# Kernel optimization log

Measured on AMD Instinct MI355X. Metric: run time of the kernel, lower is better.

## Reference

```python
import jax, jax.numpy as jnp
import numpy as np

EPS = 1e-12  # matches torch F.normalize default eps

def setup_inputs() -> dict:
    key = jax.random.key(0)
    k1, k2 = jax.random.split(key)
    n, d = 8192, 1024
    x = jax.random.normal(k1, (n, d), dtype=jnp.float32)
    weight = jax.random.normal(k2, (d, d), dtype=jnp.float32) * (2.0 / d) ** 0.5
    return {"x": x, "weight": weight}

def reference(x, weight):
    # L2-normalize rows (torch F.normalize, dim=1): x / max(||x||_2, eps)
    nrm = jnp.sqrt(jnp.sum(x * x, axis=1, keepdims=True))
    norm = x / jnp.maximum(nrm, EPS)
    # adjacency: cosine-similarity Gram matrix [n, n] (materialized as in source)
    adj = norm @ norm.T
    ax = adj @ x          # [n, d]
    axw = ax @ weight     # [n, d]
    return axw
```

## Files before the change

kernel.cpp:

```cpp
#include <hip/hip_runtime.h>
#include <stdint.h>

typedef unsigned short u16;
typedef unsigned int u32;
typedef __attribute__((ext_vector_type(8))) short short8;
typedef __attribute__((ext_vector_type(4))) float floatx4;

__device__ __forceinline__ u16 f2b(float f) {
    u32 u = __builtin_bit_cast(u32, f);
    return (u16)((u + 0x7fffu + ((u >> 16) & 1u)) >> 16);
}

__device__ __forceinline__ void gld16(const void* g, void* l) {
    __builtin_amdgcn_global_load_lds(
        (const __attribute__((address_space(1))) u32*)g,
        (__attribute__((address_space(3))) u32*)l, 16, 0, 0);
}

__global__ __launch_bounds__(256) void prep_norms(
    const float* __restrict__ x, float* __restrict__ rnorm, float* __restrict__ srnorm) {
    int row = blockIdx.x;
    int t = threadIdx.x;
    float4 v = ((const float4*)(x + (long)row * 1024))[t];
    float ss = v.x * v.x + v.y * v.y + v.z * v.z + v.w * v.w;
    #pragma unroll
    for (int off = 32; off > 0; off >>= 1) ss += __shfl_down(ss, off);
    __shared__ float red[4];
    if ((t & 63) == 0) red[t >> 6] = ss;
    __syncthreads();
    if (t == 0) {
        float r = 1.0f / fmaxf(sqrtf(red[0] + red[1] + red[2] + red[3]), 1e-12f);
        rnorm[row] = r;
        srnorm[row] = sqrtf(r);
    }
}

__global__ __launch_bounds__(256) void transpose_scale_dual(
    const float* __restrict__ src, const float* __restrict__ sr,
    u16* __restrict__ dstT, u16* __restrict__ dstR, int rows, int cols) {
    __shared__ float tile[64][65];
    __shared__ float rbuf[64];
    int r0 = blockIdx.x * 64, c0 = blockIdx.y * 64;
    int t = threadIdx.x;
    if (t < 64) rbuf[t] = (sr != nullptr) ? sr[r0 + t] : 1.0f;
    __syncthreads();
    #pragma unroll
    for (int i = 0; i < 4; i++) {
        int lin = i * 256 + t;
        int rr = lin >> 4, c4 = (lin & 15) << 2;
        float4 v = *(const float4*)(src + (long)(r0 + rr) * cols + c0 + c4);
        float s = rbuf[rr];
        v.x *= s; v.y *= s; v.z *= s; v.w *= s;
        tile[rr][c4] = v.x; tile[rr][c4 + 1] = v.y; tile[rr][c4 + 2] = v.z; tile[rr][c4 + 3] = v.w;
        if (dstR != nullptr) {
            ushort4 o; o.x = f2b(v.x); o.y = f2b(v.y); o.z = f2b(v.z); o.w = f2b(v.w);
            *(ushort4*)(dstR + (long)(r0 + rr) * cols + c0 + c4) = o;
        }
    }
    __syncthreads();
    #pragma unroll
    for (int i = 0; i < 4; i++) {
        int lin = i * 256 + t;
        int cc = lin >> 4, r4 = (lin & 15) << 2;
        ushort4 o;
        o.x = f2b(tile[r4][cc]);
        o.y = f2b(tile[r4 + 1][cc]);
        o.z = f2b(tile[r4 + 2][cc]);
        o.w = f2b(tile[r4 + 3][cc]);
        *(ushort4*)(dstT + (long)(c0 + cc) * rows + r0 + r4) = o;
    }
}

__global__ __launch_bounds__(256) void reduce_cast(
    const float* __restrict__ P, u16* __restrict__ D, int S, long E) {
    long i = ((long)blockIdx.x * 256 + threadIdx.x) * 4;
    float4 s = *(const float4*)(P + i);
    for (int z = 1; z < S; z++) {
        float4 v = *(const float4*)(P + z * E + i);
        s.x += v.x; s.y += v.y; s.z += v.z; s.w += v.w;
    }
    ushort4 o;
    o.x = f2b(s.x); o.y = f2b(s.y); o.z = f2b(s.z); o.w = f2b(s.w);
    *(ushort4*)(D + i) = o;
}

__global__ __launch_bounds__(256) void reduce_sym64(
    const float* __restrict__ P, u16* __restrict__ D, int S, long E) {
    __shared__ float lt[64][65];
    int ti = blockIdx.x >> 4, tj = blockIdx.x & 15;
    int t = threadIdx.x;
    int r = t >> 4, c4 = (t & 15) << 2;
    int kept = (ti <= 2 * (tj >> 1) + 1);
    if (kept) {
        #pragma unroll
        for (int it = 0; it < 4; it++) {
            int row = 64 * ti + it * 16 + r;
            long idx = (long)row * 1024 + 64 * tj + c4;
            float4 s = *(const float4*)(P + idx);
            for (int z = 1; z < S; z++) {
                float4 v = *(const float4*)(P + (long)z * E + idx);
                s.x += v.x; s.y += v.y; s.z += v.z; s.w += v.w;
            }
            ushort4 o; o.x = f2b(s.x); o.y = f2b(s.y); o.z = f2b(s.z); o.w = f2b(s.w);
            *(ushort4*)(D + idx) = o;
        }
    } else {
        #pragma unroll
        for (int it = 0; it < 4; it++) {
            int row = it * 16 + r;
            long idx = (long)(64 * tj + row) * 1024 + 64 * ti + c4;
            float4 s = *(const float4*)(P + idx);
            for (int z = 1; z < S; z++) {
                float4 v = *(const float4*)(P + (long)z * E + idx);
                s.x += v.x; s.y += v.y; s.z += v.z; s.w += v.w;
            }
            lt[row][c4] = s.x; lt[row][c4 + 1] = s.y; lt[row][c4 + 2] = s.z; lt[row][c4 + 3] = s.w;
        }
        __syncthreads();
        #pragma unroll
        for (int it = 0; it < 4; it++) {
            int dr = it * 16 + r;
            ushort4 o;
            o.x = f2b(lt[c4 + 0][dr]); o.y = f2b(lt[c4 + 1][dr]);
            o.z = f2b(lt[c4 + 2][dr]); o.w = f2b(lt[c4 + 3][dr]);
            *(ushort4*)(D + (long)(64 * ti + dr) * 1024 + 64 * tj + c4) = o;
        }
    }
}

__global__ __launch_bounds__(256, 4) void gemm64x128(
    const u16* __restrict__ A, const u16* __restrict__ B,
    float* __restrict__ C, const float* __restrict__ rowscale,
    int lda, int ldb, int ldc, int tilesN, int kIters, long coffz, int sym) {
    __shared__ __align__(16) u16 As[64 * 64];
    __shared__ __align__(16) u16 Bs[128 * 64];
    int tm, tn;
    if (sym) {
        int id = blockIdx.x, j = 0;
        while (true) {
            int c = (2 * j + 2 < 16) ? (2 * j + 2) : 16;
            if (id < c) break;
            id -= c; j++;
        }
        tn = j; tm = id;
    } else {
        tm = blockIdx.x / tilesN; tn = blockIdx.x % tilesN;
    }
    long kOff = (long)blockIdx.y * kIters * 64;
    const u16* Ap = A + (long)tm * 64 * lda + kOff;
    const u16* Bp = B + (long)tn * 128 * ldb + kOff;
    long coff = (long)blockIdx.y * coffz;

    int t = threadIdx.x;
    int lane = t & 63, w = t >> 6;
    int wm = (w & 1) * 32, wn = (w >> 1) * 64;
    int r16 = lane & 15, q = lane >> 4;

    int acl[2], bcl[4];
    #pragma unroll
    for (int j = 0; j < 2; j++) acl[j] = (w * 2 + j) * 64 + lane;
    #pragma unroll
    for (int j = 0; j < 4; j++) bcl[j] = (w * 4 + j) * 64 + lane;

    floatx4 acc[2][4];
    #pragma unroll
    for (int i = 0; i < 2; i++)
        #pragma unroll
        for (int j = 0; j < 4; j++) acc[i][j] = (floatx4){0.f, 0.f, 0.f, 0.f};

    for (int kt = 0; kt < kIters; kt++) {
        long kk = (long)kt * 64;
        #pragma unroll
        for (int j = 0; j < 2; j++) {
            int cl = acl[j], row = cl >> 3, cg = (cl & 7) ^ (row & 7);
            gld16(Ap + (long)row * lda + kk + cg * 8, (void*)&As[cl * 8]);
        }
        #pragma unroll
        for (int j = 0; j < 4; j++) {
            int cl = bcl[j], row = cl >> 3, cg = (cl & 7) ^ (row & 7);
            gld16(Bp + (long)row * ldb + kk + cg * 8, (void*)&Bs[cl * 8]);
        }
        __syncthreads();
        #pragma unroll
        for (int ks = 0; ks < 2; ks++) {
            short8 a[2], b[4];
            #pragma unroll
            for (int i = 0; i < 2; i++) {
                int rr = wm + i * 16 + r16;
                int cc = (ks * 4 + q) ^ (rr & 7);
                a[i] = *(const short8*)&As[rr * 64 + cc * 8];
            }
            #pragma unroll
            for (int j = 0; j < 4; j++) {
                int rr = wn + j * 16 + r16;
                int cc = (ks * 4 + q) ^ (rr & 7);
                b[j] = *(const short8*)&Bs[rr * 64 + cc * 8];
            }
            #pragma unroll
            for (int i = 0; i < 2; i++)
                #pragma unroll
                for (int j = 0; j < 4; j++)
                    acc[i][j] = __builtin_amdgcn_mfma_f32_16x16x32_bf16(a[i], b[j], acc[i][j], 0, 0, 0);
        }
        __syncthreads();
    }

    int m0 = tm * 64 + wm, n0 = tn * 128 + wn;
    #pragma unroll
    for (int i = 0; i < 2; i++) {
        int mm = m0 + i * 16 + q * 4;
        float rs[4];
        #pragma unroll
        for (int r = 0; r < 4; r++) rs[r] = (rowscale != nullptr) ? rowscale[mm + r] : 1.0f;
        #pragma unroll
        for (int j = 0; j < 4; j++) {
            int nn = n0 + j * 16 + r16;
            #pragma unroll
            for (int r = 0; r < 4; r++)
                C[coff + (long)(mm + r) * ldc + nn] = acc[i][j][r] * rs[r];
        }
    }
}

extern "C" void kernel_launch(void* const* d_in, const int* in_sizes, int n_in,
                              void* d_out, int out_size, void* d_ws, size_t ws_size,
                              hipStream_t stream) {
    const float* x = (const float*)d_in[0];
    const float* wgt = (const float*)d_in[1];
    float* out = (float*)d_out;
    char* ws = (char*)d_ws;

    const size_t MB = 1048576;
    float* rnorm  = (float*)ws;
    float* srnorm = (float*)(ws + 32768);
    u16*   YT     = (u16*)(ws + 65536);
    u16*   Yb     = (u16*)(ws + 65536 + 16 * MB);
    u16*   Wt     = (u16*)(ws + 65536 + 32 * MB);
    u16*   Gb     = (u16*)(ws + 65536 + 34 * MB);
    u16*   Mt     = (u16*)(ws + 65536 + 36 * MB);
    float* Gp     = (float*)(ws + 65536 + 38 * MB);
    float* Mp     = (float*)(ws + 65536 + 70 * MB);

    prep_norms<<<8192, 256, 0, stream>>>(x, rnorm, srnorm);
    transpose_scale_dual<<<dim3(128, 16), 256, 0, stream>>>(x, srnorm, YT, Yb, 8192, 1024);
    transpose_scale_dual<<<dim3(16, 16), 256, 0, stream>>>(wgt, nullptr, Wt, nullptr, 1024, 1024);
    gemm64x128<<<dim3(72, 8), 256, 0, stream>>>(YT, YT, Gp, nullptr,
                                                8192, 8192, 1024, 8, 16, 1048576, 1);
    reduce_sym64<<<256, 256, 0, stream>>>(Gp, Gb, 8, 1048576);
    gemm64x128<<<dim3(128, 2), 256, 0, stream>>>(Wt, Gb, Mp, nullptr,
                                                 1024, 1024, 1024, 8, 8, 1048576, 0);
    reduce_cast<<<1024, 256, 0, stream>>>(Mp, Mt, 2, 1048576);
    gemm64x128<<<dim3(1024, 1), 256, 0, stream>>>(Yb, Mt, out, srnorm,
                                                  1024, 1024, 1024, 8, 16, 0, 0);
}
```

Before: 167.6 us.

## Fuse prep kernels, store split-K partials in bf16, double split-K factors

Merges the norm computation, the bf16 cast of x and the weight transpose into a single prep kernel. The scaled transpose now reads the bf16 copy instead of the fp32 input. The split-K GEMMs write bf16 partials instead of fp32, halving partial traffic, and double their split counts (16 for the Gram matrix, 4 for W·G) to raise parallelism. The final GEMM uses the unscaled bf16 x with the full reciprocal norm as its row scale. Rounding partials to bf16 before summing adds precision loss.

After: 177.0 us. 5.6% more time.

```diff
diff --git a/kernel.cpp b/kernel.cpp
--- a/kernel.cpp
+++ b/kernel.cpp
@@ -10,52 +10,79 @@
     u32 u = __builtin_bit_cast(u32, f);
     return (u16)((u + 0x7fffu + ((u >> 16) & 1u)) >> 16);
 }
-
+__device__ __forceinline__ float b2f(u16 b) {
+    u32 u = ((u32)b) << 16;
+    return __builtin_bit_cast(float, u);
+}
 __device__ __forceinline__ void gld16(const void* g, void* l) {
     __builtin_amdgcn_global_load_lds(
         (const __attribute__((address_space(1))) u32*)g,
         (__attribute__((address_space(3))) u32*)l, 16, 0, 0);
 }
 
-__global__ __launch_bounds__(256) void prep_norms(
-    const float* __restrict__ x, float* __restrict__ rnorm, float* __restrict__ srnorm) {
-    int row = blockIdx.x;
-    int t = threadIdx.x;
-    float4 v = ((const float4*)(x + (long)row * 1024))[t];
-    float ss = v.x * v.x + v.y * v.y + v.z * v.z + v.w * v.w;
-    #pragma unroll
-    for (int off = 32; off > 0; off >>= 1) ss += __shfl_down(ss, off);
-    __shared__ float red[4];
-    if ((t & 63) == 0) red[t >> 6] = ss;
-    __syncthreads();
-    if (t == 0) {
-        float r = 1.0f / fmaxf(sqrtf(red[0] + red[1] + red[2] + red[3]), 1e-12f);
-        rnorm[row] = r;
-        srnorm[row] = sqrtf(r);
-    }
-}
-
-__global__ __launch_bounds__(256) void transpose_scale_dual(
-    const float* __restrict__ src, const float* __restrict__ sr,
-    u16* __restrict__ dstT, u16* __restrict__ dstR, int rows, int cols) {
+__global__ __launch_bounds__(256) void prep_all(
+    const float* __restrict__ x, const float* __restrict__ wgt,
+    float* __restrict__ rnorm, float* __restrict__ srnorm,
+    u16* __restrict__ xb, u16* __restrict__ Wt) {
     __shared__ float tile[64][65];
-    __shared__ float rbuf[64];
+    int bid = blockIdx.x;
+    int t = threadIdx.x;
+    if (bid < 8192) {
+        float4 v = ((const float4*)(x + (long)bid * 1024))[t];
+        float ss = v.x * v.x + v.y * v.y + v.z * v.z + v.w * v.w;
+        #pragma unroll
+        for (int off = 32; off > 0; off >>= 1) ss += __shfl_down(ss, off);
+        if ((t & 63) == 0) tile[0][t >> 6] = ss;
+        __syncthreads();
+        if (t == 0) {
+            float r = 1.0f / fmaxf(sqrtf(tile[0][0] + tile[0][1] + tile[0][2] + tile[0][3]), 1e-12f);
+            rnorm[bid] = r;
+            srnorm[bid] = sqrtf(r);
+        }
+        ushort4 o;
+        o.x = f2b(v.x); o.y = f2b(v.y); o.z = f2b(v.z); o.w = f2b(v.w);
+        *(ushort4*)(xb + (long)bid * 1024 + t * 4) = o;
+    } else {
+        int b2 = bid - 8192;
+        int r0 = (b2 >> 4) * 64, c0 = (b2 & 15) * 64;
+        #pragma unroll
+        for (int i = 0; i < 4; i++) {
+            int lin = i * 256 + t;
+            int rr = lin >> 4, c4 = (lin & 15) << 2;
+            float4 v = *(const float4*)(wgt + (long)(r0 + rr) * 1024 + c0 + c4);
+            tile[rr][c4] = v.x; tile[rr][c4 + 1] = v.y; tile[rr][c4 + 2] = v.z; tile[rr][c4 + 3] = v.w;
+        }
+        __syncthreads();
+        #pragma unroll
+        for (int i = 0; i < 4; i++) {
+            int lin = i * 256 + t;
+            int cc = lin >> 4, r4 = (lin & 15) << 2;
+            ushort4 o;
+            o.x = f2b(tile[r4][cc]);     o.y = f2b(tile[r4 + 1][cc]);
+            o.z = f2b(tile[r4 + 2][cc]); o.w = f2b(tile[r4 + 3][cc]);
+            *(ushort4*)(Wt + (long)(c0 + cc) * 1024 + r0 + r4) = o;
+        }
+    }
+}
+
+__global__ __launch_bounds__(256) void transpose_xb(
+    const u16* __restrict__ xb, const float* __restrict__ sr, u16* __restrict__ YT) {
+    __shared__ u16 tile[64][72];
+    __shared__ float rb[64];
     int r0 = blockIdx.x * 64, c0 = blockIdx.y * 64;
     int t = threadIdx.x;
-    if (t < 64) rbuf[t] = (sr != nullptr) ? sr[r0 + t] : 1.0f;
+    if (t < 64) rb[t] = sr[r0 + t];
     __syncthreads();
     #pragma unroll
     for (int i = 0; i < 4; i++) {
         int lin = i * 256 + t;
         int rr = lin >> 4, c4 = (lin & 15) << 2;
-        float4 v = *(const float4*)(src + (long)(r0 + rr) * cols + c0 + c4);
-        float s = rbuf[rr];
-        v.x *= s; v.y *= s; v.z *= s; v.w *= s;
-        tile[rr][c4] = v.x; tile[rr][c4 + 1] = v.y; tile[rr][c4 + 2] = v.z; tile[rr][c4 + 3] = v.w;
-        if (dstR != nullptr) {
-            ushort4 o; o.x = f2b(v.x); o.y = f2b(v.y); o.z = f2b(v.z); o.w = f2b(v.w);
-            *(ushort4*)(dstR + (long)(r0 + rr) * cols + c0 + c4) = o;
-        }
+        ushort4 v = *(const ushort4*)(xb + (long)(r0 + rr) * 1024 + c0 + c4);
+        float s = rb[rr];
+        tile[rr][c4]     = f2b(b2f(v.x) * s);
+        tile[rr][c4 + 1] = f2b(b2f(v.y) * s);
+        tile[rr][c4 + 2] = f2b(b2f(v.z) * s);
+        tile[rr][c4 + 3] = f2b(b2f(v.w) * s);
     }
     __syncthreads();
     #pragma unroll
@@ -63,29 +90,14 @@
         int lin = i * 256 + t;
         int cc = lin >> 4, r4 = (lin & 15) << 2;
         ushort4 o;
-        o.x = f2b(tile[r4][cc]);
-        o.y = f2b(tile[r4 + 1][cc]);
-        o.z = f2b(tile[r4 + 2][cc]);
-        o.w = f2b(tile[r4 + 3][cc]);
-        *(ushort4*)(dstT + (long)(c0 + cc) * rows + r0 + r4) = o;
-    }
-}
-
-__global__ __launch_bounds__(256) void reduce_cast(
-    const float* __restrict__ P, u16* __restrict__ D, int S, long E) {
-    long i = ((long)blockIdx.x * 256 + threadIdx.x) * 4;
-    float4 s = *(const float4*)(P + i);
-    for (int z = 1; z < S; z++) {
-        float4 v = *(const float4*)(P + z * E + i);
-        s.x += v.x; s.y += v.y; s.z += v.z; s.w += v.w;
-    }
-    ushort4 o;
-    o.x = f2b(s.x); o.y = f2b(s.y); o.z = f2b(s.z); o.w = f2b(s.w);
-    *(ushort4*)(D + i) = o;
-}
-
-__global__ __launch_bounds__(256) void reduce_sym64(
-    const float* __restrict__ P, u16* __restrict__ D, int S, long E) {
+        o.x = tile[r4][cc]; o.y = tile[r4 + 1][cc];
+        o.z = tile[r4 + 2][cc]; o.w = tile[r4 + 3][cc];
+        *(ushort4*)(YT + (long)(c0 + cc) * 8192 + r0 + r4) = o;
+    }
+}
+
+__global__ __launch_bounds__(256) void reduce_sym64_b16(
+    const u16* __restrict__ P, u16* __restrict__ D, int S, long E) {
     __shared__ float lt[64][65];
     int ti = blockIdx.x >> 4, tj = blockIdx.x & 15;
     int t = threadIdx.x;
@@ -96,12 +108,12 @@
         for (int it = 0; it < 4; it++) {
             int row = 64 * ti + it * 16 + r;
             long idx = (long)row * 1024 + 64 * tj + c4;
-            float4 s = *(const float4*)(P + idx);
-            for (int z = 1; z < S; z++) {
-                float4 v = *(const float4*)(P + (long)z * E + idx);
-                s.x += v.x; s.y += v.y; s.z += v.z; s.w += v.w;
-            }
-            ushort4 o; o.x = f2b(s.x); o.y = f2b(s.y); o.z = f2b(s.z); o.w = f2b(s.w);
+            float s0 = 0, s1 = 0, s2 = 0, s3 = 0;
+            for (int z = 0; z < S; z++) {
+                ushort4 v = *(const ushort4*)(P + (long)z * E + idx);
+                s0 += b2f(v.x); s1 += b2f(v.y); s2 += b2f(v.z); s3 += b2f(v.w);
+            }
+            ushort4 o; o.x = f2b(s0); o.y = f2b(s1); o.z = f2b(s2); o.w = f2b(s3);
             *(ushort4*)(D + idx) = o;
         }
     } else {
@@ -109,12 +121,12 @@
         for (int it = 0; it < 4; it++) {
             int row = it * 16 + r;
             long idx = (long)(64 * tj + row) * 1024 + 64 * ti + c4;
-            float4 s = *(const float4*)(P + idx);
-            for (int z = 1; z < S; z++) {
-                float4 v = *(const float4*)(P + (long)z * E + idx);
-                s.x += v.x; s.y += v.y; s.z += v.z; s.w += v.w;
-            }
-            lt[row][c4] = s.x; lt[row][c4 + 1] = s.y; lt[row][c4 + 2] = s.z; lt[row][c4 + 3] = s.w;
+            float s0 = 0, s1 = 0, s2 = 0, s3 = 0;
+            for (int z = 0; z < S; z++) {
+                ushort4 v = *(const ushort4*)(P + (long)z * E + idx);
+                s0 += b2f(v.x); s1 += b2f(v.y); s2 += b2f(v.z); s3 += b2f(v.w);
+            }
+            lt[row][c4] = s0; lt[row][c4 + 1] = s1; lt[row][c4 + 2] = s2; lt[row][c4 + 3] = s3;
         }
         __syncthreads();
         #pragma unroll
@@ -128,9 +140,21 @@
     }
 }
 
+__global__ __launch_bounds__(256) void reduce_cast_b16(
+    const u16* __restrict__ P, u16* __restrict__ D, int S, long E) {
+    long i = ((long)blockIdx.x * 256 + threadIdx.x) * 4;
+    float s0 = 0, s1 = 0, s2 = 0, s3 = 0;
+    for (int z = 0; z < S; z++) {
+        ushort4 v = *(const ushort4*)(P + (long)z * E + i);
+        s0 += b2f(v.x); s1 += b2f(v.y); s2 += b2f(v.z); s3 += b2f(v.w);
+    }
+    ushort4 o; o.x = f2b(s0); o.y = f2b(s1); o.z = f2b(s2); o.w = f2b(s3);
+    *(ushort4*)(D + i) = o;
+}
+
 __global__ __launch_bounds__(256, 4) void gemm64x128(
     const u16* __restrict__ A, const u16* __restrict__ B,
-    float* __restrict__ C, const float* __restrict__ rowscale,
+    float* __restrict__ C, u16* __restrict__ Cp, const float* __restrict__ rowscale,
     int lda, int ldb, int ldc, int tilesN, int kIters, long coffz, int sym) {
     __shared__ __align__(16) u16 As[64 * 64];
     __shared__ __align__(16) u16 Bs[128 * 64];
@@ -216,8 +240,11 @@
         for (int j = 0; j < 4; j++) {
             int nn = n0 + j * 16 + r16;
             #pragma unroll
-            for (int r = 0; r < 4; r++)
-                C[coff + (long)(mm + r) * ldc + nn] = acc[i][j][r] * rs[r];
+            for (int r = 0; r < 4; r++) {
+                long idx = (long)(mm + r) * ldc + nn;
+                if (Cp != nullptr) Cp[coff + idx] = f2b(acc[i][j][r]);
+                else               C[idx] = acc[i][j][r] * rs[r];
+            }
         }
     }
 }
@@ -233,23 +260,22 @@
     const size_t MB = 1048576;
     float* rnorm  = (float*)ws;
     float* srnorm = (float*)(ws + 32768);
-    u16*   YT     = (u16*)(ws + 65536);
-    u16*   Yb     = (u16*)(ws + 65536 + 16 * MB);
+    u16*   xb     = (u16*)(ws + 65536);
+    u16*   YT     = (u16*)(ws + 65536 + 16 * MB);
     u16*   Wt     = (u16*)(ws + 65536 + 32 * MB);
     u16*   Gb     = (u16*)(ws + 65536 + 34 * MB);
     u16*   Mt     = (u16*)(ws + 65536 + 36 * MB);
-    float* Gp     = (float*)(ws + 65536 + 38 * MB);
-    float* Mp     = (float*)(ws + 65536 + 70 * MB);
-
-    prep_norms<<<8192, 256, 0, stream>>>(x, rnorm, srnorm);
-    transpose_scale_dual<<<dim3(128, 16), 256, 0, stream>>>(x, srnorm, YT, Yb, 8192, 1024);
-    transpose_scale_dual<<<dim3(16, 16), 256, 0, stream>>>(wgt, nullptr, Wt, nullptr, 1024, 1024);
-    gemm64x128<<<dim3(72, 8), 256, 0, stream>>>(YT, YT, Gp, nullptr,
-                                                8192, 8192, 1024, 8, 16, 1048576, 1);
-    reduce_sym64<<<256, 256, 0, stream>>>(Gp, Gb, 8, 1048576);
-    gemm64x128<<<dim3(128, 2), 256, 0, stream>>>(Wt, Gb, Mp, nullptr,
-                                                 1024, 1024, 1024, 8, 8, 1048576, 0);
-    reduce_cast<<<1024, 256, 0, stream>>>(Mp, Mt, 2, 1048576);
-    gemm64x128<<<dim3(1024, 1), 256, 0, stream>>>(Yb, Mt, out, srnorm,
+    u16*   Gp     = (u16*)(ws + 65536 + 38 * MB);
+    u16*   Mp     = (u16*)(ws + 65536 + 70 * MB);
+
+    prep_all<<<8448, 256, 0, stream>>>(x, wgt, rnorm, srnorm, xb, Wt);
+    transpose_xb<<<dim3(128, 16), 256, 0, stream>>>(xb, srnorm, YT);
+    gemm64x128<<<dim3(72, 16), 256, 0, stream>>>(YT, YT, nullptr, Gp, nullptr,
+                                                 8192, 8192, 1024, 8, 8, 1048576, 1);
+    reduce_sym64_b16<<<256, 256, 0, stream>>>(Gp, Gb, 16, 1048576);
+    gemm64x128<<<dim3(128, 4), 256, 0, stream>>>(Wt, Gb, nullptr, Mp, nullptr,
+                                                 1024, 1024, 1024, 8, 4, 1048576, 0);
+    reduce_cast_b16<<<1024, 256, 0, stream>>>(Mp, Mt, 4, 1048576);
+    gemm64x128<<<dim3(1024, 1), 256, 0, stream>>>(xb, Mt, out, nullptr, rnorm,
                                                   1024, 1024, 1024, 8, 16, 0, 0);
 }
```
